# Optimization experiments

Measured on AMD Instinct MI355X. Metric: run time of the kernel, lower is better.

## Reference

```python
import jax, jax.numpy as jnp
import numpy as np

N_NODES = 50000
N_EDGES = 800000
IN_FEATS = 256
HIDDEN = 128
HEADS = 2
NEG_SLOPE = 0.2


def gat_conv(x, edge_index, W, att_src, att_dst, bias, heads, out_c, concat):
    """PyG-style GATConv: linear -> per-edge attention logits -> segment
    softmax over destination neighborhoods -> scatter-add aggregate.
    Self-loops are added (PyG default add_self_loops=True)."""
    N = x.shape[0]
    h = (x @ W.T).reshape(N, heads, out_c)           # [N,H,C]
    loop = jnp.arange(N)
    src = jnp.concatenate([edge_index[0], loop])      # [E+N]
    dst = jnp.concatenate([edge_index[1], loop])
    a_src = jnp.sum(h * att_src, axis=-1)             # [N,H]
    a_dst = jnp.sum(h * att_dst, axis=-1)
    alpha = a_src[src] + a_dst[dst]                   # [E+N,H]
    alpha = jax.nn.leaky_relu(alpha, NEG_SLOPE)
    amax = jax.ops.segment_max(alpha, dst, num_segments=N)
    alpha = jnp.exp(alpha - amax[dst])
    denom = jax.ops.segment_sum(alpha, dst, num_segments=N)
    alpha = alpha / denom[dst]
    msg = h[src] * alpha[..., None]                   # [E+N,H,C]
    out = jax.ops.segment_sum(msg, dst, num_segments=N)  # [N,H,C]
    if concat:
        out = out.reshape(N, heads * out_c)
    else:
        out = out.mean(axis=1)
    return out + bias


def setup_inputs() -> dict:
    key = jax.random.key(0)
    ks = jax.random.split(key, 12)
    x = jax.random.normal(ks[0], (N_NODES, IN_FEATS), dtype=jnp.float32)
    edge_index = jax.random.randint(ks[1], (2, N_EDGES), 0, N_NODES, dtype=jnp.int64)
    s = 0.1
    W1 = jax.random.normal(ks[2], (HEADS * HIDDEN, IN_FEATS), dtype=jnp.float32) * s
    att_src1 = jax.random.normal(ks[3], (1, HEADS, HIDDEN), dtype=jnp.float32) * s
    att_dst1 = jax.random.normal(ks[4], (1, HEADS, HIDDEN), dtype=jnp.float32) * s
    b1 = jnp.zeros((HEADS * HIDDEN,), dtype=jnp.float32)
    W2 = jax.random.normal(ks[5], (HIDDEN, HEADS * HIDDEN), dtype=jnp.float32) * s
    att_src2 = jax.random.normal(ks[6], (1, 1, HIDDEN), dtype=jnp.float32) * s
    att_dst2 = jax.random.normal(ks[7], (1, 1, HIDDEN), dtype=jnp.float32) * s
    b2 = jnp.zeros((HIDDEN,), dtype=jnp.float32)
    return {"x": x, "edge_index": edge_index,
            "W1": W1, "att_src1": att_src1, "att_dst1": att_dst1, "b1": b1,
            "W2": W2, "att_src2": att_src2, "att_dst2": att_dst2, "b2": b2}


def reference(x, edge_index, W1, att_src1, att_dst1, b1, W2, att_src2, att_dst2, b2):
    h = gat_conv(x, edge_index, W1, att_src1, att_dst1, b1, HEADS, HIDDEN, True)
    h = jax.nn.relu(h)
    out = gat_conv(h, edge_index, W2, att_src2, att_dst2, b2, 1, HIDDEN, False)
    return out
```

## Files before the change

kernel.cpp:

```cpp
#include <hip/hip_runtime.h>
#include <hip/hip_bf16.h>


typedef _Float16 half8v __attribute__((ext_vector_type(8)));
typedef _Float16 half4v __attribute__((ext_vector_type(4)));
typedef _Float16 half2v __attribute__((ext_vector_type(2)));
typedef float f32x4 __attribute__((ext_vector_type(4)));


template <typename TA, int H, bool SCATTER>
__global__ __launch_bounds__(256) void gemm_att_kernel(
    const TA* __restrict__ A,
    const float* __restrict__ B,
    _Float16* __restrict__ C,
    const float* __restrict__ att_s,
    const float* __restrict__ att_d,
    float* __restrict__ a_s,
    float* __restrict__ a_d,
    int M, int K, int GB,
    const int* __restrict__ esrc, const int* __restrict__ edst,
    const int* __restrict__ rank, const int* __restrict__ csr_off,
    int* __restrict__ csr_src, int E, int nScatBlk)
{
    constexpr int BM = 128, BK = 32, LDA = 40;
    constexpr int NCOL = H * 128;
    __shared__ _Float16 Ah[BM * LDA];
    __shared__ _Float16 Bh[BM * LDA];
    __shared__ float red[2][2][64][2];

    const int tid = threadIdx.x;
    const int bid = blockIdx.x;

    if constexpr (SCATTER) {
        if (bid >= GB * H) {
            const int sbid = bid - GB * H;
            const int nq = (E + 3) >> 2;
            for (int q = sbid * 256 + tid; q < nq; q += nScatBlk * 256) {
                const int e4 = q * 4;
                if (e4 + 3 < E) {
                    const int4 sv = *reinterpret_cast<const int4*>(esrc + e4);
                    const int4 dv = *reinterpret_cast<const int4*>(edst + e4);
                    const int4 rv = *reinterpret_cast<const int4*>(rank + e4);
                    csr_src[csr_off[dv.x] + 1 + rv.x] = sv.x;
                    csr_src[csr_off[dv.y] + 1 + rv.y] = sv.y;
                    csr_src[csr_off[dv.z] + 1 + rv.z] = sv.z;
                    csr_src[csr_off[dv.w] + 1 + rv.w] = sv.w;
                } else {
                    for (int k = e4; k < E; ++k)
                        csr_src[csr_off[edst[k]] + 1 + rank[k]] = esrc[k];
                }
            }
            return;
        }
    }

    const int m0 = (bid % GB) * BM;
    const int by = bid / GB;
    const int n0 = by * 128;
    const int w  = tid >> 6;
    const int l  = tid & 63;
    const int wm = (w >> 1) * 64;
    const int wn = (w & 1) * 64;
    const int lr = l & 15;
    const int lq = l >> 4;

    f32x4 acc[4][4] = {};

    for (int k0 = 0; k0 < K; k0 += BK) {
        if constexpr (__is_same(TA, float)) {
#pragma unroll
            for (int it = 0; it < 4; ++it) {
                const int row = (tid >> 3) + it * 32;
                const int gm  = min(m0 + row, M - 1);
                const int c4  = (tid & 7) * 4;
                float4 v = *reinterpret_cast<const float4*>(A + (long)gm * K + k0 + c4);
                half4v o = { (_Float16)v.x, (_Float16)v.y, (_Float16)v.z, (_Float16)v.w };
                *reinterpret_cast<half4v*>(&Ah[row * LDA + c4]) = o;
            }
        } else {
#pragma unroll
            for (int it = 0; it < 2; ++it) {
                const int row = (tid >> 2) + it * 64;
                const int gm  = min(m0 + row, M - 1);
                const int c8  = (tid & 3) * 8;
                float4 v = *reinterpret_cast<const float4*>((const char*)A + ((long)gm * K + k0 + c8) * 2);
                *reinterpret_cast<float4*>(&Ah[row * LDA + c8]) = v;
            }
        }
#pragma unroll
        for (int it = 0; it < 4; ++it) {
            const int row = (tid >> 3) + it * 32;
            const int c4  = (tid & 7) * 4;
            float4 v = *reinterpret_cast<const float4*>(B + (long)(n0 + row) * K + k0 + c4);
            half4v o = { (_Float16)v.x, (_Float16)v.y, (_Float16)v.z, (_Float16)v.w };
            *reinterpret_cast<half4v*>(&Bh[row * LDA + c4]) = o;
        }
        __syncthreads();

        half8v af[4], bf[4];
#pragma unroll
        for (int i = 0; i < 4; ++i)
            af[i] = *reinterpret_cast<const half8v*>(&Ah[(wm + i * 16 + lr) * LDA + lq * 8]);
#pragma unroll
        for (int j = 0; j < 4; ++j)
            bf[j] = *reinterpret_cast<const half8v*>(&Bh[(wn + j * 16 + lr) * LDA + lq * 8]);
#pragma unroll
        for (int i = 0; i < 4; ++i)
#pragma unroll
            for (int j = 0; j < 4; ++j)
                acc[i][j] = __builtin_amdgcn_mfma_f32_16x16x32_f16(af[i], bf[j], acc[i][j], 0, 0, 0);
        __syncthreads();
    }

#pragma unroll
    for (int i = 0; i < 4; ++i) {
        const int gm_base = m0 + wm + i * 16 + lq * 4;
#pragma unroll
        for (int r = 0; r < 4; ++r) {
            const int gm = gm_base + r;
            if (gm < M) {
#pragma unroll
                for (int j = 0; j < 4; ++j)
                    C[(long)gm * NCOL + n0 + wn + j * 16 + lr] = (_Float16)acc[i][j][r];
            }
        }
    }

    float asv[4], adv[4];
#pragma unroll
    for (int j = 0; j < 4; ++j) {
        asv[j] = att_s[n0 + wn + j * 16 + lr];
        adv[j] = att_d[n0 + wn + j * 16 + lr];
    }
    float ps[4][4] = {}, pd[4][4] = {};
#pragma unroll
    for (int i = 0; i < 4; ++i)
#pragma unroll
        for (int j = 0; j < 4; ++j)
#pragma unroll
            for (int r = 0; r < 4; ++r) {
                ps[i][r] += acc[i][j][r] * asv[j];
                pd[i][r] += acc[i][j][r] * adv[j];
            }
#pragma unroll
    for (int o = 1; o < 16; o <<= 1)
#pragma unroll
        for (int i = 0; i < 4; ++i)
#pragma unroll
            for (int r = 0; r < 4; ++r) {
                ps[i][r] += __shfl_xor(ps[i][r], o, 64);
                pd[i][r] += __shfl_xor(pd[i][r], o, 64);
            }
    if (lr == 0) {
#pragma unroll
        for (int i = 0; i < 4; ++i)
#pragma unroll
            for (int r = 0; r < 4; ++r) {
                const int row = i * 16 + lq * 4 + r;
                red[wm >> 6][wn >> 6][row][0] = ps[i][r];
                red[wm >> 6][wn >> 6][row][1] = pd[i][r];
            }
    }
    __syncthreads();
    if (wn == 0) {
        const int row = l;
        const int gm = m0 + wm + row;
        if (gm < M) {
            const int wi = wm >> 6;
            a_s[(long)gm * H + by] = red[wi][0][row][0] + red[wi][1][row][0];
            a_d[(long)gm * H + by] = red[wi][0][row][1] + red[wi][1][row][1];
        }
    }
}


__global__ void count_kernel(const int* __restrict__ dst, int* __restrict__ deg,
                             int* __restrict__ rank, int E)
{
    const int tid = blockIdx.x * blockDim.x + threadIdx.x;
    const int e4 = tid * 4;
    if (e4 + 3 < E) {
        const int4 d = *reinterpret_cast<const int4*>(dst + e4);
        int4 r;
        r.x = atomicAdd(&deg[d.x], 1);
        r.y = atomicAdd(&deg[d.y], 1);
        r.z = atomicAdd(&deg[d.z], 1);
        r.w = atomicAdd(&deg[d.w], 1);
        *reinterpret_cast<int4*>(rank + e4) = r;
    } else if (e4 < E) {
        for (int k = e4; k < E; ++k) rank[k] = atomicAdd(&deg[dst[k]], 1);
    }
}

__global__ __launch_bounds__(256) void block_scan_kernel(
    const int* __restrict__ deg, int* __restrict__ pre, int* __restrict__ blk, int n)
{
    __shared__ int s[256];
    const int t = threadIdx.x;
    const int base = blockIdx.x * 1024 + t * 4;
    int4 d = make_int4(-1, -1, -1, -1);
    if (base + 3 < n) d = *reinterpret_cast<const int4*>(deg + base);
    else {
        if (base + 0 < n) d.x = deg[base + 0];
        if (base + 1 < n) d.y = deg[base + 1];
        if (base + 2 < n) d.z = deg[base + 2];
        if (base + 3 < n) d.w = deg[base + 3];
    }
    const int v0 = d.x + 1, v1 = d.y + 1, v2 = d.z + 1, v3 = d.w + 1;
    s[t] = v0 + v1 + v2 + v3;
    __syncthreads();
#pragma unroll
    for (int o = 1; o < 256; o <<= 1) {
        int val = 0;
        if (t >= o) val = s[t - o];
        __syncthreads();
        s[t] += val;
        __syncthreads();
    }
    int run = (t == 0) ? 0 : s[t - 1];
    int4 o4;
    o4.x = run; run += v0;
    o4.y = run; run += v1;
    o4.z = run; run += v2;
    o4.w = run; run += v3;
    if (base + 3 < n) *reinterpret_cast<int4*>(pre + base) = o4;
    else {
        if (base + 0 < n) pre[base + 0] = o4.x;
        if (base + 1 < n) pre[base + 1] = o4.y;
        if (base + 2 < n) pre[base + 2] = o4.z;
        if (base + 3 < n) pre[base + 3] = o4.w;
    }
    if (t == 255) blk[blockIdx.x] = s[255];
}

__global__ __launch_bounds__(256) void finalize_scan_kernel(
    const int* __restrict__ pre, const int* __restrict__ blk,
    int* __restrict__ off, int* __restrict__ csr_src, int n, int nvb)
{
    __shared__ int s_add;
    const int vb = blockIdx.x;
    const int t  = threadIdx.x;
    if (t < 64) {
        int v = (t < vb) ? blk[t] : 0;
#pragma unroll
        for (int o = 32; o > 0; o >>= 1) v += __shfl_xor(v, o, 64);
        if (t == 0) s_add = v;
    }
    __syncthreads();
    const int add = s_add;
    const int base = vb * 1024 + t * 4;
    if (base + 3 < n) {
        int4 p = *reinterpret_cast<const int4*>(pre + base);
        p.x += add; p.y += add; p.z += add; p.w += add;
        *reinterpret_cast<int4*>(off + base) = p;
        csr_src[p.x] = base + 0;
        csr_src[p.y] = base + 1;
        csr_src[p.z] = base + 2;
        csr_src[p.w] = base + 3;
    } else {
#pragma unroll
        for (int k = 0; k < 4; ++k)
            if (base + k < n) {
                const int v = pre[base + k] + add;
                off[base + k] = v;
                csr_src[v] = base + k;
            }
    }
    if (vb == nvb - 1 && t == 0) off[n] = add + blk[vb];
}


#define AGG_TILE 64

template <int H, int C, int VPT, bool RELU, typename TOUT>
__global__ __launch_bounds__(H * C / VPT) void aggregate_kernel(
    const int* __restrict__ csr_off,
    const int* __restrict__ csr_src,
    const _Float16* __restrict__ h,
    const float* __restrict__ a_s,
    const float* __restrict__ a_d,
    const float* __restrict__ bias,
    TOUT* __restrict__ out)
{
    const int d   = blockIdx.x;
    const int t   = threadIdx.x;
    const int col = t * VPT;
    const int hh  = col / C;

    __shared__ int   s_src[AGG_TILE];
    __shared__ float s_w[AGG_TILE][H];

    const int beg = csr_off[d];
    const int end = csr_off[d + 1];

    float acc[VPT] = {};
    float wsum = 0.f;

    for (int base = beg; base < end; base += AGG_TILE) {
        const int len = min(AGG_TILE, end - base);
        if (t < len) {
            const int s = csr_src[base + t];
            s_src[t] = s;
#pragma unroll
            for (int h2 = 0; h2 < H; ++h2) {
                float logit = a_s[s * H + h2] + a_d[d * H + h2];
                logit = logit > 0.f ? logit : 0.2f * logit;
                s_w[t][h2] = __expf(logit);
            }
        }
        __syncthreads();
#pragma unroll 4
        for (int j = 0; j < len; ++j) {
            const float w = s_w[j][hh];
            const int   s = s_src[j];
            if constexpr (VPT == 4) {
                half4v hv = *reinterpret_cast<const half4v*>(h + (long)s * (H * C) + col);
                acc[0] += w * (float)hv.x;
                acc[1] += w * (float)hv.y;
                acc[2] += w * (float)hv.z;
                acc[3] += w * (float)hv.w;
            } else {
                half2v hv = *reinterpret_cast<const half2v*>(h + (long)s * (H * C) + col);
                acc[0] += w * (float)hv.x;
                acc[1] += w * (float)hv.y;
            }
            wsum += w;
        }
        __syncthreads();
    }

    const float inv = 1.f / wsum;
    float r[VPT];
#pragma unroll
    for (int k = 0; k < VPT; ++k) {
        r[k] = acc[k] * inv + bias[col + k];
        if (RELU) r[k] = r[k] > 0.f ? r[k] : 0.f;
    }
    if constexpr (__is_same(TOUT, _Float16)) {
#pragma unroll
        for (int k = 0; k < VPT; ++k)
            out[(long)d * (H * C) + col + k] = (_Float16)r[k];
    } else {
#pragma unroll
        for (int k = 0; k < VPT; ++k)
            out[(long)d * (H * C) + col + k] = r[k];
    }
}


extern "C" void kernel_launch(void* const* d_in, const int* in_sizes, int n_in,
                              void* d_out, int out_size, void* d_ws, size_t ws_size,
                              hipStream_t stream)
{
    const float* x    = (const float*)d_in[0];
    const int*   eidx = (const int*)d_in[1];
    const float* W1   = (const float*)d_in[2];
    const float* as1  = (const float*)d_in[3];
    const float* ad1  = (const float*)d_in[4];
    const float* b1   = (const float*)d_in[5];
    const float* W2   = (const float*)d_in[6];
    const float* as2  = (const float*)d_in[7];
    const float* ad2  = (const float*)d_in[8];
    const float* b2   = (const float*)d_in[9];
    float* out = (float*)d_out;

    const int IN_FEATS = 256;
    const int N = in_sizes[0] / IN_FEATS;
    const int E = in_sizes[1] / 2;

    const int* esrc = eidx;
    const int* edst = eidx + E;

    size_t off = 0;
    auto alloc = [&](size_t bytes) -> void* {
        void* p = (char*)d_ws + off;
        off += (bytes + 255) & ~(size_t)255;
        return p;
    };
    _Float16* h1h   = (_Float16*)alloc((size_t)N * 256 * 2);
    _Float16* o1h   = (_Float16*)alloc((size_t)N * 256 * 2);
    _Float16* h2h   = (_Float16*)alloc((size_t)N * 128 * 2);
    float* a1s      = (float*)alloc((size_t)N * 2 * 4);
    float* a1d      = (float*)alloc((size_t)N * 2 * 4);
    float* a2s      = (float*)alloc((size_t)N * 4);
    float* a2d      = (float*)alloc((size_t)N * 4);
    int*   deg      = (int*)alloc((size_t)N * 4);
    int*   pre      = (int*)alloc((size_t)N * 4);
    int*   rank     = (int*)alloc((size_t)E * 4);
    int*   csr_off  = (int*)alloc((size_t)(N + 1) * 4);
    int*   csr_src  = (int*)alloc((size_t)(E + N) * 4);
    int*   blk      = (int*)alloc(64 * 4);

    const int nvb = (N + 1023) / 1024;

    hipMemsetAsync(deg, 0, (size_t)N * 4, stream);
    count_kernel<<<((E + 3) / 4 + 255) / 256, 256, 0, stream>>>(edst, deg, rank, E);
    block_scan_kernel<<<nvb, 256, 0, stream>>>(deg, pre, blk, N);
    finalize_scan_kernel<<<nvb, 256, 0, stream>>>(pre, blk, csr_off, csr_src, N, nvb);

    {
        const int GB = (N + 127) / 128;
        const int nScat = 192;
        gemm_att_kernel<float, 2, true><<<GB * 2 + nScat, 256, 0, stream>>>(
            x, W1, h1h, as1, ad1, a1s, a1d, N, 256, GB,
            esrc, edst, rank, csr_off, csr_src, E, nScat);
    }
    aggregate_kernel<2, 128, 4, true, _Float16><<<N, 64, 0, stream>>>(
        csr_off, csr_src, h1h, a1s, a1d, b1, o1h);

    {
        const int GB = (N + 127) / 128;
        gemm_att_kernel<_Float16, 1, false><<<GB, 256, 0, stream>>>(
            o1h, W2, h2h, as2, ad2, a2s, a2d, N, 256, GB,
            nullptr, nullptr, nullptr, nullptr, nullptr, 0, 0);
    }
    aggregate_kernel<1, 128, 2, false, float><<<N, 64, 0, stream>>>(
        csr_off, csr_src, h2h, a2s, a2d, b2, out);
}
```

Baseline: 291.8 us.

## Restructure aggregation to one wavefront per node with edge-parallel lane groups

The aggregation kernel now packs four destination nodes per 256-thread block, giving each 64-lane wavefront one node, and replaces block-wide __syncthreads with wave barriers. Each lane loads 8 halves (16-byte loads), and the lanes are split into groups that process different edges at once. The groups' partial sums are combined with xor-shuffles at the end. The source index and weight are packed together in shared memory, and a_d is hoisted out of the loop. This targets the small-block launch overhead and the narrow per-edge gathers, at the cost of a shuffle reduction and padded edge slots.

Result: no change. 292.7 us (+0.3%).

```diff
diff --git a/kernel.cpp b/kernel.cpp
--- a/kernel.cpp
+++ b/kernel.cpp
@@ -270,80 +270,109 @@
 }
 
 
-#define AGG_TILE 64
-
-template <int H, int C, int VPT, bool RELU, typename TOUT>
-__global__ __launch_bounds__(H * C / VPT) void aggregate_kernel(
+template <int H, int C, bool RELU, typename TOUT>
+__global__ __launch_bounds__(256) void aggregate_kernel(
     const int* __restrict__ csr_off,
     const int* __restrict__ csr_src,
     const _Float16* __restrict__ h,
     const float* __restrict__ a_s,
     const float* __restrict__ a_d,
     const float* __restrict__ bias,
-    TOUT* __restrict__ out)
-{
-    const int d   = blockIdx.x;
-    const int t   = threadIdx.x;
-    const int col = t * VPT;
+    TOUT* __restrict__ out,
+    int N)
+{
+    constexpr int VPT = 8;
+    constexpr int HC  = H * C;
+    constexpr int LPE = HC / VPT;
+    constexpr int GRP = 64 / LPE;
+
+    const int w = threadIdx.x >> 6;
+    const int l = threadIdx.x & 63;
+    const int d = blockIdx.x * 4 + w;
+    if (d >= N) return;
+
+    const int g   = l / LPE;
+    const int col = (l % LPE) * VPT;
     const int hh  = col / C;
 
-    __shared__ int   s_src[AGG_TILE];
-    __shared__ float s_w[AGG_TILE][H];
+    __shared__ float2 s_sw[4][64][H];
 
     const int beg = csr_off[d];
     const int end = csr_off[d + 1];
 
+    float ad0 = 0.f, ad1 = 0.f;
+    if constexpr (H == 2) {
+        const float2 t2 = *reinterpret_cast<const float2*>(a_d + (long)d * 2);
+        ad0 = t2.x; ad1 = t2.y;
+    } else {
+        ad0 = a_d[d];
+    }
+
     float acc[VPT] = {};
     float wsum = 0.f;
 
-    for (int base = beg; base < end; base += AGG_TILE) {
-        const int len = min(AGG_TILE, end - base);
-        if (t < len) {
-            const int s = csr_src[base + t];
-            s_src[t] = s;
-#pragma unroll
-            for (int h2 = 0; h2 < H; ++h2) {
-                float logit = a_s[s * H + h2] + a_d[d * H + h2];
-                logit = logit > 0.f ? logit : 0.2f * logit;
-                s_w[t][h2] = __expf(logit);
-            }
-        }
-        __syncthreads();
-#pragma unroll 4
-        for (int j = 0; j < len; ++j) {
-            const float w = s_w[j][hh];
-            const int   s = s_src[j];
-            if constexpr (VPT == 4) {
-                half4v hv = *reinterpret_cast<const half4v*>(h + (long)s * (H * C) + col);
-                acc[0] += w * (float)hv.x;
-                acc[1] += w * (float)hv.y;
-                acc[2] += w * (float)hv.z;
-                acc[3] += w * (float)hv.w;
+    for (int base = beg; base < end; base += 64) {
+        const int len  = min(64, end - base);
+        const int lenp = (len + GRP - 1) & ~(GRP - 1);
+        if (l < len) {
+            const int s = csr_src[base + l];
+            if constexpr (H == 2) {
+                const float2 sv = *reinterpret_cast<const float2*>(a_s + (long)s * 2);
+                float lg0 = sv.x + ad0; lg0 = lg0 > 0.f ? lg0 : 0.2f * lg0;
+                float lg1 = sv.y + ad1; lg1 = lg1 > 0.f ? lg1 : 0.2f * lg1;
+                s_sw[w][l][0] = make_float2(__int_as_float(s), __expf(lg0));
+                s_sw[w][l][1] = make_float2(__int_as_float(s), __expf(lg1));
             } else {
-                half2v hv = *reinterpret_cast<const half2v*>(h + (long)s * (H * C) + col);
-                acc[0] += w * (float)hv.x;
-                acc[1] += w * (float)hv.y;
-            }
-            wsum += w;
-        }
-        __syncthreads();
-    }
-
-    const float inv = 1.f / wsum;
-    float r[VPT];
-#pragma unroll
-    for (int k = 0; k < VPT; ++k) {
-        r[k] = acc[k] * inv + bias[col + k];
-        if (RELU) r[k] = r[k] > 0.f ? r[k] : 0.f;
-    }
-    if constexpr (__is_same(TOUT, _Float16)) {
-#pragma unroll
-        for (int k = 0; k < VPT; ++k)
-            out[(long)d * (H * C) + col + k] = (_Float16)r[k];
-    } else {
-#pragma unroll
-        for (int k = 0; k < VPT; ++k)
-            out[(long)d * (H * C) + col + k] = r[k];
+                float lg = a_s[s] + ad0; lg = lg > 0.f ? lg : 0.2f * lg;
+                s_sw[w][l][0] = make_float2(__int_as_float(s), __expf(lg));
+            }
+        } else if (l < lenp) {
+#pragma unroll
+            for (int h2 = 0; h2 < H; ++h2)
+                s_sw[w][l][h2] = make_float2(__int_as_float(d), 0.f);
+        }
+        __builtin_amdgcn_wave_barrier();
+#pragma unroll 2
+        for (int jj = 0; jj < lenp; jj += GRP) {
+            const float2 sw = s_sw[w][jj + g][hh];
+            const int    s  = __float_as_int(sw.x);
+            const float  wt = sw.y;
+            const half8v hv = *reinterpret_cast<const half8v*>(
+                h + (long)s * HC + col);
+#pragma unroll
+            for (int k = 0; k < VPT; ++k)
+                acc[k] += wt * (float)hv[k];
+            wsum += wt;
+        }
+        __builtin_amdgcn_wave_barrier();
+    }
+
+#pragma unroll
+    for (int o = LPE; o < 64; o <<= 1) {
+#pragma unroll
+        for (int k = 0; k < VPT; ++k) acc[k] += __shfl_xor(acc[k], o, 64);
+        wsum += __shfl_xor(wsum, o, 64);
+    }
+
+    if (g == 0) {
+        const float inv = 1.f / wsum;
+        float r[VPT];
+#pragma unroll
+        for (int k = 0; k < VPT; ++k) {
+            r[k] = acc[k] * inv + bias[col + k];
+            if (RELU) r[k] = r[k] > 0.f ? r[k] : 0.f;
+        }
+        if constexpr (__is_same(TOUT, _Float16)) {
+            half8v ov;
+#pragma unroll
+            for (int k = 0; k < VPT; ++k) ov[k] = (_Float16)r[k];
+            *reinterpret_cast<half8v*>(out + (long)d * HC + col) = ov;
+        } else {
+            f32x4 o0 = { r[0], r[1], r[2], r[3] };
+            f32x4 o1 = { r[4], r[5], r[6], r[7] };
+            *reinterpret_cast<f32x4*>(out + (long)d * HC + col)     = o0;
+            *reinterpret_cast<f32x4*>(out + (long)d * HC + col + 4) = o1;
+        }
     }
 }
 
@@ -405,8 +434,8 @@
             x, W1, h1h, as1, ad1, a1s, a1d, N, 256, GB,
             esrc, edst, rank, csr_off, csr_src, E, nScat);
     }
-    aggregate_kernel<2, 128, 4, true, _Float16><<<N, 64, 0, stream>>>(
-        csr_off, csr_src, h1h, a1s, a1d, b1, o1h);
+    aggregate_kernel<2, 128, true, _Float16><<<(N + 3) / 4, 256, 0, stream>>>(
+        csr_off, csr_src, h1h, a1s, a1d, b1, o1h, N);
 
     {
         const int GB = (N + 127) / 128;
@@ -414,6 +443,6 @@
             o1h, W2, h2h, as2, ad2, a2s, a2d, N, 256, GB,
             nullptr, nullptr, nullptr, nullptr, nullptr, 0, 0);
     }
-    aggregate_kernel<1, 128, 2, false, float><<<N, 64, 0, stream>>>(
-        csr_off, csr_src, h2h, a2s, a2d, b2, out);
-}
+    aggregate_kernel<1, 128, false, float><<<(N + 3) / 4, 256, 0, stream>>>(
+        csr_off, csr_src, h2h, a2s, a2d, b2, out, N);
+}
```
